# Optimization experiments

Hardware: AMD Instinct MI355X
Metric: run time of the kernel (lower is better)

Reference implementation:

```python
import jax, jax.numpy as jnp
import numpy as np

B, IDF, CDF, H, Wd, L = 16, 128, 256, 128, 128, 64


def setup_inputs() -> dict:
    key = jax.random.key(0)
    k1, k2, k3, k4 = jax.random.split(key, 4)
    x = jax.random.normal(k1, (B, IDF, H, Wd), dtype=jnp.float32)
    context = jax.random.normal(k2, (B, CDF, L), dtype=jnp.float32)
    W = jax.random.normal(k3, (IDF, CDF), dtype=jnp.float32) * 0.02
    mask = jax.random.bernoulli(k4, 0.3, (B, L))
    # guarantee at least one unmasked word per row so the softmax is finite
    mask = mask.at[:, 0].set(False)
    return {"x": x, "context": context, "W": W, "mask": mask}


def reference(x, context, W, mask):
    # x: [B, idf, H, W]  context: [B, cdf, L]  W: [idf, cdf]  mask: [B, L] bool
    b, c, h, w = x.shape
    P = h * w
    l = context.shape[2]
    target = x.reshape(b, c, P)                       # [B, idf, P]
    # Conv1x1 over context (cdf -> idf)
    source = jnp.einsum('oc,bcl->bol', W, context)    # [B, idf, L]
    # QK^T: [B, P, idf] x [B, idf, L] -> [B, P, L]
    attn = jnp.einsum('bip,bil->bpl', target, source)
    attn = attn.reshape(b * P, l)
    # faithful to torch: mask.repeat(P, 1) tiled over the flattened rows
    m = jnp.tile(mask, (P, 1))                        # [B*P, L]
    attn = jnp.where(m, -jnp.inf, attn)
    attn = jax.nn.softmax(attn, axis=1).reshape(b, P, l)
    attnT = jnp.swapaxes(attn, 1, 2)                  # [B, L, P]
    # weighted context: [B, idf, L] x [B, L, P] -> [B, idf, P]
    weight = jnp.einsum('bil,blp->bip', source, attnT).reshape(b, c, h, w)
    attn_out = attnT.reshape(b, l, h, w)
    return weight, attn_out
```

## Files before the change

kernel.cpp:

```cpp
#include <hip/hip_runtime.h>
#include <hip/hip_bf16.h>
#include <hip/hip_fp16.h>

#define NB  16
#define IDF 128
#define CDF 256
#define LL  64
#define PP  16384
#define PXB 256
#define XPITCH 260

typedef _Float16 f16;
typedef _Float16 f16x4 __attribute__((ext_vector_type(4)));
typedef _Float16 f16x8 __attribute__((ext_vector_type(8)));
typedef float    f32x4 __attribute__((ext_vector_type(4)));

__global__ void src_pack_kernel(const float* __restrict__ Wm,
                                const float* __restrict__ ctx,
                                f16* __restrict__ srcF,
                                f16* __restrict__ srcT,
                                const unsigned char* __restrict__ mask_raw,
                                unsigned long long* __restrict__ mbits) {
    if (blockIdx.x == 0) {
        __shared__ int is_u8;
        const int tid = threadIdx.x;
        if (tid == 0) is_u8 = 0;
        if (tid < 16) mbits[tid] = 0ULL;
        __syncthreads();
        unsigned char byt[4];
        #pragma unroll
        for (int q = 0; q < 4; ++q) {
            int k = tid + q * 256;
            byt[q] = mask_raw[k];
            if ((k & 3) != 0 && byt[q] != 0) atomicOr(&is_u8, 1);
        }
        __syncthreads();
        #pragma unroll
        for (int q = 0; q < 4; ++q) {
            int k = tid + q * 256;
            int masked;
            if (is_u8) masked = (byt[q] != 0);
            else       masked = (((const int*)mask_raw)[k] != 0);
            if (masked) atomicOr(&mbits[k >> 6], 1ULL << (unsigned)(k & 63));
        }
    }

    int g = blockIdx.x * 256 + threadIdx.x;
    int l = g & (LL - 1);
    int i = (g >> 6) & (IDF - 1);
    int b = g >> 13;
    const float* wrow = Wm + (size_t)i * CDF;
    const float* ccol = ctx + (size_t)b * CDF * LL + l;
    float s = 0.f;
    #pragma unroll 8
    for (int c = 0; c < CDF; ++c)
        s = fmaf(wrow[c], ccol[(size_t)c * LL], s);
    f16 h = (f16)s;
    srcF[g] = h;
    srcT[((size_t)b * LL + l) * IDF + i] = h;
}

__global__ __launch_bounds__(256, 2)
void attn_mfma_kernel(const float* __restrict__ x,
                      const f16* __restrict__ srcT,
                      const f16* __restrict__ srcF,
                      const unsigned long long* __restrict__ mbits,
                      float* __restrict__ weight,
                      float* __restrict__ attn_out) {
    __shared__ __align__(16) unsigned char s_srcT[LL * 256];
    __shared__ __align__(16) unsigned char s_srcF[IDF * 128];
    __shared__ __align__(16) unsigned char s_u[34816];

    float* s_xpA = (float*)s_u;
    float* s_xpB = (float*)(s_u + 16640);

    const int b    = blockIdx.y;
    const int tid  = threadIdx.x;
    const int wv   = tid >> 6;
    const int lane = tid & 63;
    const int c    = lane & 15;
    const int g    = lane >> 4;
    const int cs   = (c & 7) << 4;

    f16* s_pw = (f16*)s_u + (size_t)wv * (64 * 68);

    const int bxs = (blockIdx.x & 7) * 8 + (blockIdx.x >> 3);
    const int pwb = bxs * PXB;
    const int pww = pwb + wv * 64;
    const float* xb = x + (size_t)b * IDF * PP + pww + c;

    unsigned mlo[4], mhi[4];
    #pragma unroll
    for (int r = 0; r < 4; ++r) {
        unsigned long long m = mbits[4 * g + r];
        mlo[r] = (unsigned)m;
        mhi[r] = (unsigned)(m >> 32);
    }

    float xfa[32], xfb[32];
#define QK_LOAD(BUF, KS)                                                    \
    {   _Pragma("unroll")                                                   \
        for (int pt = 0; pt < 4; ++pt)                                      \
            _Pragma("unroll")                                               \
            for (int j = 0; j < 8; ++j)                                     \
                BUF[pt * 8 + j] =                                           \
                    xb[(size_t)((KS) * 32 + 8 * g + j) * PP + pt * 16];     \
    }

    QK_LOAD(xfa, 0)

    {
        const f16* sT = srcT + (size_t)b * LL * IDF;
        const f16* sF = srcF + (size_t)b * IDF * LL;
        #pragma unroll
        for (int it = 0; it < 4; ++it) {
            int e = (it * 256 + tid) * 8;
            int l = e >> 7, i = e & 127;
            f16x8 v = *reinterpret_cast<const f16x8*>(sT + l * IDF + i);
            *reinterpret_cast<f16x8*>(
                s_srcT + l * 256 + ((i * 2) ^ ((l & 7) << 4))) = v;
        }
        #pragma unroll
        for (int it = 0; it < 4; ++it) {
            int e = (it * 256 + tid) * 8;
            int i = e >> 6, l = e & 63;
            f16x8 v = *reinterpret_cast<const f16x8*>(sF + i * LL + l);
            *reinterpret_cast<f16x8*>(
                s_srcF + i * 128 + ((l * 2) ^ ((i & 7) << 4))) = v;
        }
    }
    __syncthreads();

    f32x4 acc[4][4];
    #pragma unroll
    for (int pt = 0; pt < 4; ++pt)
        #pragma unroll
        for (int nt = 0; nt < 4; ++nt) acc[pt][nt] = (f32x4){0.f, 0.f, 0.f, 0.f};

#define QK_STEP(BUF, KS)                                                    \
    {   f16x8 xa[4];                                                        \
        _Pragma("unroll")                                                   \
        for (int pt = 0; pt < 4; ++pt)                                      \
            _Pragma("unroll")                                               \
            for (int j = 0; j < 8; ++j) xa[pt][j] = (f16)BUF[pt * 8 + j];   \
        _Pragma("unroll")                                                   \
        for (int nt = 0; nt < 4; ++nt) {                                    \
            const f16x8 bt = *reinterpret_cast<const f16x8*>(               \
                s_srcT + (nt * 16 + c) * 256 + (((KS) * 64 + 16 * g) ^ cs));\
            _Pragma("unroll")                                               \
            for (int pt = 0; pt < 4; ++pt)                                  \
                acc[pt][nt] = __builtin_amdgcn_mfma_f32_16x16x32_f16(       \
                    xa[pt], bt, acc[pt][nt], 0, 0, 0);                      \
        } }

    QK_LOAD(xfb, 1)
    QK_STEP(xfa, 0)
    QK_LOAD(xfa, 2)
    QK_STEP(xfb, 1)
    QK_LOAD(xfb, 3)
    QK_STEP(xfa, 2)
    QK_STEP(xfb, 3)

    #pragma unroll
    for (int r = 0; r < 4; ++r) {
        const unsigned m0 = (mlo[r] >> c) & 1u;
        const unsigned m1 = (mlo[r] >> (16 + c)) & 1u;
        const unsigned m2 = (mhi[r] >> c) & 1u;
        const unsigned m3 = (mhi[r] >> (16 + c)) & 1u;
        #pragma unroll
        for (int pt = 0; pt < 4; ++pt) {
            if (m0) acc[pt][0][r] = -INFINITY;
            if (m1) acc[pt][1][r] = -INFINITY;
            if (m2) acc[pt][2][r] = -INFINITY;
            if (m3) acc[pt][3][r] = -INFINITY;
        }
    }
    #pragma unroll
    for (int pt = 0; pt < 4; ++pt) {
        #pragma unroll
        for (int r = 0; r < 4; ++r) {
            float mx = fmaxf(fmaxf(acc[pt][0][r], acc[pt][1][r]),
                             fmaxf(acc[pt][2][r], acc[pt][3][r]));
            mx = fmaxf(mx, __shfl_xor(mx, 1, 64));
            mx = fmaxf(mx, __shfl_xor(mx, 2, 64));
            mx = fmaxf(mx, __shfl_xor(mx, 4, 64));
            mx = fmaxf(mx, __shfl_xor(mx, 8, 64));
            float sum = 0.f;
            #pragma unroll
            for (int nt = 0; nt < 4; ++nt) {
                float e = exp2f((acc[pt][nt][r] - mx) * 1.44269504f);
                acc[pt][nt][r] = e;
                sum += e;
            }
            sum += __shfl_xor(sum, 1, 64);
            sum += __shfl_xor(sum, 2, 64);
            sum += __shfl_xor(sum, 4, 64);
            sum += __shfl_xor(sum, 8, 64);
            const float inv = 1.f / sum;
            #pragma unroll
            for (int nt = 0; nt < 4; ++nt) acc[pt][nt][r] *= inv;
        }
    }

    #pragma unroll
    for (int pt = 0; pt < 4; ++pt)
        #pragma unroll
        for (int nt = 0; nt < 4; ++nt)
            #pragma unroll
            for (int r = 0; r < 4; ++r)
                s_pw[(pt * 16 + 4 * g + r) * 68 + nt * 16 + c] =
                    (f16)acc[pt][nt][r];

    f16x8 pa[4][2];
    #pragma unroll
    for (int pt = 0; pt < 4; ++pt)
        #pragma unroll
        for (int ks = 0; ks < 2; ++ks) {
            const f16* pp = s_pw + (pt * 16 + c) * 68 + ks * 32 + 8 * g;
            f16x4 lo = *reinterpret_cast<const f16x4*>(pp);
            f16x4 hi = *reinterpret_cast<const f16x4*>(pp + 4);
            f16x8 v;
            #pragma unroll
            for (int j = 0; j < 4; ++j) { v[j] = lo[j]; v[4 + j] = hi[j]; }
            pa[pt][ks] = v;
        }

    __syncthreads();

    float* abase = attn_out + (size_t)b * LL * PP + pwb;
    float* wbase = weight + (size_t)b * IDF * PP + pwb;

#define FILL_ATTN(NT, XP)                                                   \
    {   _Pragma("unroll")                                                   \
        for (int pt = 0; pt < 4; ++pt)                                      \
            *reinterpret_cast<f32x4*>(                                      \
                (XP) + c * XPITCH + wv * 64 + pt * 16 + 4 * g) = acc[pt][NT]; }

#define FILL_PV(CH, XP)                                                     \
    {   f32x4 a2[4];                                                        \
        _Pragma("unroll")                                                   \
        for (int pt = 0; pt < 4; ++pt) a2[pt] = (f32x4){0.f, 0.f, 0.f, 0.f};\
        _Pragma("unroll")                                                   \
        for (int ks = 0; ks < 2; ++ks) {                                    \
            const f16x8 sf = *reinterpret_cast<const f16x8*>(               \
                s_srcF + ((CH) * 16 + c) * 128 + ((ks * 64 + 16 * g) ^ cs));\
            _Pragma("unroll")                                               \
            for (int pt = 0; pt < 4; ++pt)                                  \
                a2[pt] = __builtin_amdgcn_mfma_f32_16x16x32_f16(            \
                    pa[pt][ks], sf, a2[pt], 0, 0, 0);                       \
        }                                                                   \
        _Pragma("unroll")                                                   \
        for (int pt = 0; pt < 4; ++pt)                                      \
            *reinterpret_cast<f32x4*>(                                      \
                (XP) + c * XPITCH + wv * 64 + pt * 16 + 4 * g) = a2[pt]; }

#define FILL_CHUNK(K, XP)                                                   \
    {   if ((K) < 4) { FILL_ATTN((K), (XP)) }                               \
        else         { FILL_PV((K) - 4, (XP)) } }

#define STORE_CHUNK(K, XP)                                                  \
    {   float* dst = ((K) < 4)                                              \
            ? (abase + (size_t)((K) * 16) * PP)                             \
            : (wbase + (size_t)(((K) - 4) * 16) * PP);                      \
        _Pragma("unroll")                                                   \
        for (int k2 = 0; k2 < 4; ++k2) {                                    \
            int f = tid + k2 * 256;                                         \
            int row = f >> 6, u = f & 63;                                   \
            f32x4 v = *reinterpret_cast<const f32x4*>(                      \
                (XP) + row * XPITCH + u * 4);                               \
            __builtin_nontemporal_store(v,                                  \
                reinterpret_cast<f32x4*>(dst + (size_t)row * PP + u * 4));  \
        } }

    FILL_CHUNK(0, s_xpA)
    __syncthreads();
    #pragma unroll
    for (int k = 0; k < 12; ++k) {
        float* xp_cur = (k & 1) ? s_xpB : s_xpA;
        float* xp_nxt = (k & 1) ? s_xpA : s_xpB;
        STORE_CHUNK(k, xp_cur)
        if (k < 11) { FILL_CHUNK(k + 1, xp_nxt) }
        if (k < 11) __syncthreads();
    }
}

extern "C" void kernel_launch(void* const* d_in, const int* in_sizes, int n_in,
                              void* d_out, int out_size, void* d_ws, size_t ws_size,
                              hipStream_t stream) {
    const float*         x        = (const float*)d_in[0];
    const float*         ctx      = (const float*)d_in[1];
    const float*         Wm       = (const float*)d_in[2];
    const unsigned char* mask_raw = (const unsigned char*)d_in[3];

    float* weight   = (float*)d_out;
    float* attn_out = weight + (size_t)NB * IDF * PP;

    unsigned long long* mbits = (unsigned long long*)d_ws;
    f16* srcF = (f16*)((char*)d_ws + 4096);
    f16* srcT = srcF + (size_t)NB * IDF * LL;

    src_pack_kernel<<<(NB * IDF * LL) / 256, 256, 0, stream>>>(
        Wm, ctx, srcF, srcT, mask_raw, mbits);

    dim3 grid(PP / PXB, NB);
    attn_mfma_kernel<<<grid, 256, 0, stream>>>(x, srcT, srcF, mbits, weight, attn_out);
}
```

Measured before the change: 77.10 us.

## Process two pixel tiles per block and prefetch second tile's x during stores

Each block now handles two consecutive 256-pixel tiles, which halves the grid and reuses the staged source matrices in LDS. The second tile's x loads are issued in the middle of the first tile's store pipeline, so global reads overlap with the output writes. __syncthreads is replaced by an explicit lgkmcnt wait plus s_barrier, so outstanding global stores are not drained at each barrier. The cost is fewer blocks (512 total), which may hurt occupancy or load balance, and more live registers for the prefetched data.

```diff
diff --git a/kernel.cpp b/kernel.cpp
--- a/kernel.cpp
+++ b/kernel.cpp
@@ -14,6 +14,9 @@
 typedef _Float16 f16x4 __attribute__((ext_vector_type(4)));
 typedef _Float16 f16x8 __attribute__((ext_vector_type(8)));
 typedef float    f32x4 __attribute__((ext_vector_type(4)));
+
+#define BAR() do { asm volatile("s_waitcnt lgkmcnt(0)" ::: "memory"); \
+                   __builtin_amdgcn_s_barrier(); } while (0)
 
 __global__ void src_pack_kernel(const float* __restrict__ Wm,
                                 const float* __restrict__ ctx,
@@ -84,10 +87,10 @@
 
     f16* s_pw = (f16*)s_u + (size_t)wv * (64 * 68);
 
-    const int bxs = (blockIdx.x & 7) * 8 + (blockIdx.x >> 3);
-    const int pwb = bxs * PXB;
-    const int pww = pwb + wv * 64;
-    const float* xb = x + (size_t)b * IDF * PP + pww + c;
+    const int bxs = (blockIdx.x & 7) * 4 + (blockIdx.x >> 3);
+    const int pwb = bxs * (2 * PXB);
+    const float* xb0 = x + (size_t)b * IDF * PP + pwb + wv * 64 + c;
+    const float* xb1 = xb0 + PXB;
 
     unsigned mlo[4], mhi[4];
     #pragma unroll
@@ -98,16 +101,159 @@
     }
 
     float xfa[32], xfb[32];
-#define QK_LOAD(BUF, KS)                                                    \
+    f16x8 xh0[4], xh1[4];
+    f32x4 acc[4][4];
+    f16x8 pa[4][2];
+
+#define QK_LOAD(BUF, KS, XB)                                                \
     {   _Pragma("unroll")                                                   \
         for (int pt = 0; pt < 4; ++pt)                                      \
             _Pragma("unroll")                                               \
             for (int j = 0; j < 8; ++j)                                     \
                 BUF[pt * 8 + j] =                                           \
-                    xb[(size_t)((KS) * 32 + 8 * g + j) * PP + pt * 16];     \
-    }
-
-    QK_LOAD(xfa, 0)
+                    (XB)[(size_t)((KS) * 32 + 8 * g + j) * PP + pt * 16];   \
+    }
+
+#define QK_CONV(BUF, XH)                                                    \
+    {   _Pragma("unroll")                                                   \
+        for (int pt = 0; pt < 4; ++pt)                                      \
+            _Pragma("unroll")                                               \
+            for (int j = 0; j < 8; ++j) XH[pt][j] = (f16)BUF[pt * 8 + j];   \
+    }
+
+#define QK_STEP_H(XH, KS)                                                   \
+    {   _Pragma("unroll")                                                   \
+        for (int nt = 0; nt < 4; ++nt) {                                    \
+            const f16x8 bt = *reinterpret_cast<const f16x8*>(               \
+                s_srcT + (nt * 16 + c) * 256 + (((KS) * 64 + 16 * g) ^ cs));\
+            _Pragma("unroll")                                               \
+            for (int pt = 0; pt < 4; ++pt)                                  \
+                acc[pt][nt] = __builtin_amdgcn_mfma_f32_16x16x32_f16(       \
+                    XH[pt], bt, acc[pt][nt], 0, 0, 0);                      \
+        } }
+
+#define QK_STEP(BUF, KS)                                                    \
+    {   f16x8 xa_[4];                                                       \
+        QK_CONV(BUF, xa_)                                                   \
+        QK_STEP_H(xa_, KS) }
+
+#define ACC_ZERO()                                                          \
+    {   _Pragma("unroll")                                                   \
+        for (int pt = 0; pt < 4; ++pt)                                      \
+            _Pragma("unroll")                                               \
+            for (int nt = 0; nt < 4; ++nt)                                  \
+                acc[pt][nt] = (f32x4){0.f, 0.f, 0.f, 0.f}; }
+
+#define SOFTMAX()                                                           \
+    {   _Pragma("unroll")                                                   \
+        for (int r = 0; r < 4; ++r) {                                       \
+            const unsigned m0 = (mlo[r] >> c) & 1u;                         \
+            const unsigned m1 = (mlo[r] >> (16 + c)) & 1u;                  \
+            const unsigned m2 = (mhi[r] >> c) & 1u;                         \
+            const unsigned m3 = (mhi[r] >> (16 + c)) & 1u;                  \
+            _Pragma("unroll")                                               \
+            for (int pt = 0; pt < 4; ++pt) {                                \
+                if (m0) acc[pt][0][r] = -INFINITY;                          \
+                if (m1) acc[pt][1][r] = -INFINITY;                          \
+                if (m2) acc[pt][2][r] = -INFINITY;                          \
+                if (m3) acc[pt][3][r] = -INFINITY;                          \
+            }                                                               \
+        }                                                                   \
+        _Pragma("unroll")                                                   \
+        for (int pt = 0; pt < 4; ++pt) {                                    \
+            _Pragma("unroll")                                               \
+            for (int r = 0; r < 4; ++r) {                                   \
+                float mx = fmaxf(fmaxf(acc[pt][0][r], acc[pt][1][r]),       \
+                                 fmaxf(acc[pt][2][r], acc[pt][3][r]));      \
+                mx = fmaxf(mx, __shfl_xor(mx, 1, 64));                      \
+                mx = fmaxf(mx, __shfl_xor(mx, 2, 64));                      \
+                mx = fmaxf(mx, __shfl_xor(mx, 4, 64));                      \
+                mx = fmaxf(mx, __shfl_xor(mx, 8, 64));                      \
+                float sum = 0.f;                                            \
+                _Pragma("unroll")                                           \
+                for (int nt = 0; nt < 4; ++nt) {                            \
+                    float e = exp2f((acc[pt][nt][r] - mx) * 1.44269504f);   \
+                    acc[pt][nt][r] = e;                                     \
+                    sum += e;                                               \
+                }                                                           \
+                sum += __shfl_xor(sum, 1, 64);                              \
+                sum += __shfl_xor(sum, 2, 64);                              \
+                sum += __shfl_xor(sum, 4, 64);                              \
+                sum += __shfl_xor(sum, 8, 64);                              \
+                const float inv = 1.f / sum;                                \
+                _Pragma("unroll")                                           \
+                for (int nt = 0; nt < 4; ++nt) acc[pt][nt][r] *= inv;       \
+            }                                                               \
+        } }
+
+#define PROB_EXCHANGE()                                                     \
+    {   _Pragma("unroll")                                                   \
+        for (int pt = 0; pt < 4; ++pt)                                      \
+            _Pragma("unroll")                                               \
+            for (int nt = 0; nt < 4; ++nt)                                  \
+                _Pragma("unroll")                                           \
+                for (int r = 0; r < 4; ++r)                                 \
+                    s_pw[(pt * 16 + 4 * g + r) * 68 + nt * 16 + c] =        \
+                        (f16)acc[pt][nt][r];                                \
+        _Pragma("unroll")                                                   \
+        for (int pt = 0; pt < 4; ++pt)                                      \
+            _Pragma("unroll")                                               \
+            for (int ks = 0; ks < 2; ++ks) {                                \
+                const f16* pp = s_pw + (pt * 16 + c) * 68 + ks * 32 + 8 * g;\
+                f16x4 lo = *reinterpret_cast<const f16x4*>(pp);             \
+                f16x4 hi = *reinterpret_cast<const f16x4*>(pp + 4);         \
+                f16x8 v;                                                    \
+                _Pragma("unroll")                                           \
+                for (int j = 0; j < 4; ++j) { v[j] = lo[j]; v[4+j] = hi[j]; } \
+                pa[pt][ks] = v;                                             \
+            } }
+
+#define FILL_ATTN(NT, XP)                                                   \
+    {   _Pragma("unroll")                                                   \
+        for (int pt = 0; pt < 4; ++pt)                                      \
+            *reinterpret_cast<f32x4*>(                                      \
+                (XP) + c * XPITCH + wv * 64 + pt * 16 + 4 * g) = acc[pt][NT]; }
+
+#define FILL_PV(CH, XP)                                                     \
+    {   f32x4 a2[4];                                                        \
+        _Pragma("unroll")                                                   \
+        for (int pt = 0; pt < 4; ++pt) a2[pt] = (f32x4){0.f, 0.f, 0.f, 0.f};\
+        _Pragma("unroll")                                                   \
+        for (int ks = 0; ks < 2; ++ks) {                                    \
+            const f16x8 sf = *reinterpret_cast<const f16x8*>(               \
+                s_srcF + ((CH) * 16 + c) * 128 + ((ks * 64 + 16 * g) ^ cs));\
+            _Pragma("unroll")                                               \
+            for (int pt = 0; pt < 4; ++pt)                                  \
+                a2[pt] = __builtin_amdgcn_mfma_f32_16x16x32_f16(            \
+                    pa[pt][ks], sf, a2[pt], 0, 0, 0);                       \
+        }                                                                   \
+        _Pragma("unroll")                                                   \
+        for (int pt = 0; pt < 4; ++pt)                                      \
+            *reinterpret_cast<f32x4*>(                                      \
+                (XP) + c * XPITCH + wv * 64 + pt * 16 + 4 * g) = a2[pt]; }
+
+#define FILL_CHUNK(K, XP)                                                   \
+    {   if ((K) < 4) { FILL_ATTN((K), (XP)) }                               \
+        else         { FILL_PV((K) - 4, (XP)) } }
+
+#define STORE_CHUNK(K, XP, AB, WB)                                          \
+    {   float* dst = ((K) < 4)                                              \
+            ? ((AB) + (size_t)((K) * 16) * PP)                              \
+            : ((WB) + (size_t)(((K) - 4) * 16) * PP);                       \
+        _Pragma("unroll")                                                   \
+        for (int k2 = 0; k2 < 4; ++k2) {                                    \
+            int f = tid + k2 * 256;                                         \
+            int row = f >> 6, u = f & 63;                                   \
+            f32x4 v = *reinterpret_cast<const f32x4*>(                      \
+                (XP) + row * XPITCH + u * 4);                               \
+            __builtin_nontemporal_store(v,                                  \
+                reinterpret_cast<f32x4*>(dst + (size_t)row * PP + u * 4));  \
+        } }
+
+#define PIPE_STEP(K, CUR, NXT, AB, WB)                                      \
+    STORE_CHUNK(K, CUR, AB, WB) FILL_CHUNK((K) + 1, NXT) BAR();
+
+    QK_LOAD(xfa, 0, xb0)
 
     {
         const f16* sT = srcT + (size_t)b * LL * IDF;
@@ -129,159 +275,70 @@
                 s_srcF + i * 128 + ((l * 2) ^ ((i & 7) << 4))) = v;
         }
     }
-    __syncthreads();
-
-    f32x4 acc[4][4];
-    #pragma unroll
-    for (int pt = 0; pt < 4; ++pt)
-        #pragma unroll
-        for (int nt = 0; nt < 4; ++nt) acc[pt][nt] = (f32x4){0.f, 0.f, 0.f, 0.f};
-
-#define QK_STEP(BUF, KS)                                                    \
-    {   f16x8 xa[4];                                                        \
-        _Pragma("unroll")                                                   \
-        for (int pt = 0; pt < 4; ++pt)                                      \
-            _Pragma("unroll")                                               \
-            for (int j = 0; j < 8; ++j) xa[pt][j] = (f16)BUF[pt * 8 + j];   \
-        _Pragma("unroll")                                                   \
-        for (int nt = 0; nt < 4; ++nt) {                                    \
-            const f16x8 bt = *reinterpret_cast<const f16x8*>(               \
-                s_srcT + (nt * 16 + c) * 256 + (((KS) * 64 + 16 * g) ^ cs));\
-            _Pragma("unroll")                                               \
-            for (int pt = 0; pt < 4; ++pt)                                  \
-                acc[pt][nt] = __builtin_amdgcn_mfma_f32_16x16x32_f16(       \
-                    xa[pt], bt, acc[pt][nt], 0, 0, 0);                      \
-        } }
-
-    QK_LOAD(xfb, 1)
+    BAR();
+
+    ACC_ZERO()
+    QK_LOAD(xfb, 1, xb0)
     QK_STEP(xfa, 0)
-    QK_LOAD(xfa, 2)
+    QK_LOAD(xfa, 2, xb0)
     QK_STEP(xfb, 1)
-    QK_LOAD(xfb, 3)
+    QK_LOAD(xfb, 3, xb0)
     QK_STEP(xfa, 2)
     QK_STEP(xfb, 3)
-
-    #pragma unroll
-    for (int r = 0; r < 4; ++r) {
-        const unsigned m0 = (mlo[r] >> c) & 1u;
-        const unsigned m1 = (mlo[r] >> (16 + c)) & 1u;
-        const unsigned m2 = (mhi[r] >> c) & 1u;
-        const unsigned m3 = (mhi[r] >> (16 + c)) & 1u;
-        #pragma unroll
-        for (int pt = 0; pt < 4; ++pt) {
-            if (m0) acc[pt][0][r] = -INFINITY;
-            if (m1) acc[pt][1][r] = -INFINITY;
-            if (m2) acc[pt][2][r] = -INFINITY;
-            if (m3) acc[pt][3][r] = -INFINITY;
-        }
-    }
-    #pragma unroll
-    for (int pt = 0; pt < 4; ++pt) {
-        #pragma unroll
-        for (int r = 0; r < 4; ++r) {
-            float mx = fmaxf(fmaxf(acc[pt][0][r], acc[pt][1][r]),
-                             fmaxf(acc[pt][2][r], acc[pt][3][r]));
-            mx = fmaxf(mx, __shfl_xor(mx, 1, 64));
-            mx = fmaxf(mx, __shfl_xor(mx, 2, 64));
-            mx = fmaxf(mx, __shfl_xor(mx, 4, 64));
-            mx = fmaxf(mx, __shfl_xor(mx, 8, 64));
-            float sum = 0.f;
-            #pragma unroll
-            for (int nt = 0; nt < 4; ++nt) {
-                float e = exp2f((acc[pt][nt][r] - mx) * 1.44269504f);
-                acc[pt][nt][r] = e;
-                sum += e;
-            }
-            sum += __shfl_xor(sum, 1, 64);
-            sum += __shfl_xor(sum, 2, 64);
-            sum += __shfl_xor(sum, 4, 64);
-            sum += __shfl_xor(sum, 8, 64);
-            const float inv = 1.f / sum;
-            #pragma unroll
-            for (int nt = 0; nt < 4; ++nt) acc[pt][nt][r] *= inv;
-        }
-    }
-
-    #pragma unroll
-    for (int pt = 0; pt < 4; ++pt)
-        #pragma unroll
-        for (int nt = 0; nt < 4; ++nt)
-            #pragma unroll
-            for (int r = 0; r < 4; ++r)
-                s_pw[(pt * 16 + 4 * g + r) * 68 + nt * 16 + c] =
-                    (f16)acc[pt][nt][r];
-
-    f16x8 pa[4][2];
-    #pragma unroll
-    for (int pt = 0; pt < 4; ++pt)
-        #pragma unroll
-        for (int ks = 0; ks < 2; ++ks) {
-            const f16* pp = s_pw + (pt * 16 + c) * 68 + ks * 32 + 8 * g;
-            f16x4 lo = *reinterpret_cast<const f16x4*>(pp);
-            f16x4 hi = *reinterpret_cast<const f16x4*>(pp + 4);
-            f16x8 v;
-            #pragma unroll
-            for (int j = 0; j < 4; ++j) { v[j] = lo[j]; v[4 + j] = hi[j]; }
-            pa[pt][ks] = v;
-        }
-
-    __syncthreads();
-
-    float* abase = attn_out + (size_t)b * LL * PP + pwb;
-    float* wbase = weight + (size_t)b * IDF * PP + pwb;
-
-#define FILL_ATTN(NT, XP)                                                   \
-    {   _Pragma("unroll")                                                   \
-        for (int pt = 0; pt < 4; ++pt)                                      \
-            *reinterpret_cast<f32x4*>(                                      \
-                (XP) + c * XPITCH + wv * 64 + pt * 16 + 4 * g) = acc[pt][NT]; }
-
-#define FILL_PV(CH, XP)                                                     \
-    {   f32x4 a2[4];                                                        \
-        _Pragma("unroll")                                                   \
-        for (int pt = 0; pt < 4; ++pt) a2[pt] = (f32x4){0.f, 0.f, 0.f, 0.f};\
-        _Pragma("unroll")                                                   \
-        for (int ks = 0; ks < 2; ++ks) {                                    \
-            const f16x8 sf = *reinterpret_cast<const f16x8*>(               \
-                s_srcF + ((CH) * 16 + c) * 128 + ((ks * 64 + 16 * g) ^ cs));\
-            _Pragma("unroll")                                               \
-            for (int pt = 0; pt < 4; ++pt)                                  \
-                a2[pt] = __builtin_amdgcn_mfma_f32_16x16x32_f16(            \
-                    pa[pt][ks], sf, a2[pt], 0, 0, 0);                       \
-        }                                                                   \
-        _Pragma("unroll")                                                   \
-        for (int pt = 0; pt < 4; ++pt)                                      \
-            *reinterpret_cast<f32x4*>(                                      \
-                (XP) + c * XPITCH + wv * 64 + pt * 16 + 4 * g) = a2[pt]; }
-
-#define FILL_CHUNK(K, XP)                                                   \
-    {   if ((K) < 4) { FILL_ATTN((K), (XP)) }                               \
-        else         { FILL_PV((K) - 4, (XP)) } }
-
-#define STORE_CHUNK(K, XP)                                                  \
-    {   float* dst = ((K) < 4)                                              \
-            ? (abase + (size_t)((K) * 16) * PP)                             \
-            : (wbase + (size_t)(((K) - 4) * 16) * PP);                      \
-        _Pragma("unroll")                                                   \
-        for (int k2 = 0; k2 < 4; ++k2) {                                    \
-            int f = tid + k2 * 256;                                         \
-            int row = f >> 6, u = f & 63;                                   \
-            f32x4 v = *reinterpret_cast<const f32x4*>(                      \
-                (XP) + row * XPITCH + u * 4);                               \
-            __builtin_nontemporal_store(v,                                  \
-                reinterpret_cast<f32x4*>(dst + (size_t)row * PP + u * 4));  \
-        } }
+    SOFTMAX()
+    PROB_EXCHANGE()
+    BAR();
+
+    float* abase0 = attn_out + (size_t)b * LL * PP + pwb;
+    float* wbase0 = weight + (size_t)b * IDF * PP + pwb;
+    float* abase1 = abase0 + PXB;
+    float* wbase1 = wbase0 + PXB;
 
     FILL_CHUNK(0, s_xpA)
-    __syncthreads();
-    #pragma unroll
-    for (int k = 0; k < 12; ++k) {
-        float* xp_cur = (k & 1) ? s_xpB : s_xpA;
-        float* xp_nxt = (k & 1) ? s_xpA : s_xpB;
-        STORE_CHUNK(k, xp_cur)
-        if (k < 11) { FILL_CHUNK(k + 1, xp_nxt) }
-        if (k < 11) __syncthreads();
-    }
+    BAR();
+    PIPE_STEP(0, s_xpA, s_xpB, abase0, wbase0)
+    PIPE_STEP(1, s_xpB, s_xpA, abase0, wbase0)
+    PIPE_STEP(2, s_xpA, s_xpB, abase0, wbase0)
+    QK_LOAD(xfa, 0, xb1)
+    QK_LOAD(xfb, 1, xb1)
+    PIPE_STEP(3, s_xpB, s_xpA, abase0, wbase0)
+    PIPE_STEP(4, s_xpA, s_xpB, abase0, wbase0)
+    PIPE_STEP(5, s_xpB, s_xpA, abase0, wbase0)
+    PIPE_STEP(6, s_xpA, s_xpB, abase0, wbase0)
+    QK_CONV(xfa, xh0)
+    QK_CONV(xfb, xh1)
+    QK_LOAD(xfa, 2, xb1)
+    QK_LOAD(xfb, 3, xb1)
+    PIPE_STEP(7, s_xpB, s_xpA, abase0, wbase0)
+    PIPE_STEP(8, s_xpA, s_xpB, abase0, wbase0)
+    PIPE_STEP(9, s_xpB, s_xpA, abase0, wbase0)
+    PIPE_STEP(10, s_xpA, s_xpB, abase0, wbase0)
+    STORE_CHUNK(11, s_xpB, abase0, wbase0)
+    BAR();
+
+    ACC_ZERO()
+    QK_STEP_H(xh0, 0)
+    QK_STEP_H(xh1, 1)
+    QK_STEP(xfa, 2)
+    QK_STEP(xfb, 3)
+    SOFTMAX()
+    PROB_EXCHANGE()
+    BAR();
+
+    FILL_CHUNK(0, s_xpA)
+    BAR();
+    PIPE_STEP(0, s_xpA, s_xpB, abase1, wbase1)
+    PIPE_STEP(1, s_xpB, s_xpA, abase1, wbase1)
+    PIPE_STEP(2, s_xpA, s_xpB, abase1, wbase1)
+    PIPE_STEP(3, s_xpB, s_xpA, abase1, wbase1)
+    PIPE_STEP(4, s_xpA, s_xpB, abase1, wbase1)
+    PIPE_STEP(5, s_xpB, s_xpA, abase1, wbase1)
+    PIPE_STEP(6, s_xpA, s_xpB, abase1, wbase1)
+    PIPE_STEP(7, s_xpB, s_xpA, abase1, wbase1)
+    PIPE_STEP(8, s_xpA, s_xpB, abase1, wbase1)
+    PIPE_STEP(9, s_xpB, s_xpA, abase1, wbase1)
+    PIPE_STEP(10, s_xpA, s_xpB, abase1, wbase1)
+    STORE_CHUNK(11, s_xpB, abase1, wbase1)
 }
 
 extern "C" void kernel_launch(void* const* d_in, const int* in_sizes, int n_in,
@@ -302,6 +359,6 @@
     src_pack_kernel<<<(NB * IDF * LL) / 256, 256, 0, stream>>>(
         Wm, ctx, srcF, srcT, mask_raw, mbits);
 
-    dim3 grid(PP / PXB, NB);
+    dim3 grid(PP / (2 * PXB), NB);
     attn_mfma_kernel<<<grid, 256, 0, stream>>>(x, srcT, srcF, mbits, weight, attn_out);
 }
```

After: 77.78 us. About the same (+0.9%).

## Single-buffer LDS staging and raise occupancy to three blocks per CU

Applied to the files above, without the earlier changes.

Shrinks the shared staging area from a double buffer to a single buffer and shrinks the per-wave probability scratch by staging P in two halves. This lowers LDS per block so launch bounds can request three blocks per CU. It also replaces __syncthreads with a custom barrier that only waits on LDS counters, not global loads or stores. The cost is an extra barrier per output chunk, since fill and store no longer overlap, and tighter register limits that may cause spills.

```diff
diff --git a/kernel.cpp b/kernel.cpp
--- a/kernel.cpp
+++ b/kernel.cpp
@@ -14,6 +14,9 @@
 typedef _Float16 f16x4 __attribute__((ext_vector_type(4)));
 typedef _Float16 f16x8 __attribute__((ext_vector_type(8)));
 typedef float    f32x4 __attribute__((ext_vector_type(4)));
+
+#define BAR() do { asm volatile("s_waitcnt lgkmcnt(0)" ::: "memory"); \
+                   __builtin_amdgcn_s_barrier(); } while (0)
 
 __global__ void src_pack_kernel(const float* __restrict__ Wm,
                                 const float* __restrict__ ctx,
@@ -60,7 +63,7 @@
     srcT[((size_t)b * LL + l) * IDF + i] = h;
 }
 
-__global__ __launch_bounds__(256, 2)
+__global__ __launch_bounds__(256, 3)
 void attn_mfma_kernel(const float* __restrict__ x,
                       const f16* __restrict__ srcT,
                       const f16* __restrict__ srcF,
@@ -69,10 +72,9 @@
                       float* __restrict__ attn_out) {
     __shared__ __align__(16) unsigned char s_srcT[LL * 256];
     __shared__ __align__(16) unsigned char s_srcF[IDF * 128];
-    __shared__ __align__(16) unsigned char s_u[34816];
-
-    float* s_xpA = (float*)s_u;
-    float* s_xpB = (float*)(s_u + 16640);
+    __shared__ __align__(16) unsigned char s_u[17408];
+
+    float* s_xp = (float*)s_u;
 
     const int b    = blockIdx.y;
     const int tid  = threadIdx.x;
@@ -82,7 +84,7 @@
     const int g    = lane >> 4;
     const int cs   = (c & 7) << 4;
 
-    f16* s_pw = (f16*)s_u + (size_t)wv * (64 * 68);
+    f16* s_pw = (f16*)(s_u + (size_t)wv * 4352);
 
     const int bxs = (blockIdx.x & 7) * 8 + (blockIdx.x >> 3);
     const int pwb = bxs * PXB;
@@ -98,6 +100,9 @@
     }
 
     float xfa[32], xfb[32];
+    f32x4 acc[4][4];
+    f16x8 pa[4][2];
+
 #define QK_LOAD(BUF, KS)                                                    \
     {   _Pragma("unroll")                                                   \
         for (int pt = 0; pt < 4; ++pt)                                      \
@@ -107,6 +112,22 @@
                     xb[(size_t)((KS) * 32 + 8 * g + j) * PP + pt * 16];     \
     }
 
+#define QK_STEP(BUF, KS)                                                    \
+    {   f16x8 xa_[4];                                                       \
+        _Pragma("unroll")                                                   \
+        for (int pt = 0; pt < 4; ++pt)                                      \
+            _Pragma("unroll")                                               \
+            for (int j = 0; j < 8; ++j) xa_[pt][j] = (f16)BUF[pt * 8 + j];  \
+        _Pragma("unroll")                                                   \
+        for (int nt = 0; nt < 4; ++nt) {                                    \
+            const f16x8 bt = *reinterpret_cast<const f16x8*>(               \
+                s_srcT + (nt * 16 + c) * 256 + (((KS) * 64 + 16 * g) ^ cs));\
+            _Pragma("unroll")                                               \
+            for (int pt = 0; pt < 4; ++pt)                                  \
+                acc[pt][nt] = __builtin_amdgcn_mfma_f32_16x16x32_f16(       \
+                    xa_[pt], bt, acc[pt][nt], 0, 0, 0);                     \
+        } }
+
     QK_LOAD(xfa, 0)
 
     {
@@ -129,29 +150,12 @@
                 s_srcF + i * 128 + ((l * 2) ^ ((i & 7) << 4))) = v;
         }
     }
-    __syncthreads();
-
-    f32x4 acc[4][4];
+    BAR();
+
     #pragma unroll
     for (int pt = 0; pt < 4; ++pt)
         #pragma unroll
         for (int nt = 0; nt < 4; ++nt) acc[pt][nt] = (f32x4){0.f, 0.f, 0.f, 0.f};
-
-#define QK_STEP(BUF, KS)                                                    \
-    {   f16x8 xa[4];                                                        \
-        _Pragma("unroll")                                                   \
-        for (int pt = 0; pt < 4; ++pt)                                      \
-            _Pragma("unroll")                                               \
-            for (int j = 0; j < 8; ++j) xa[pt][j] = (f16)BUF[pt * 8 + j];   \
-        _Pragma("unroll")                                                   \
-        for (int nt = 0; nt < 4; ++nt) {                                    \
-            const f16x8 bt = *reinterpret_cast<const f16x8*>(               \
-                s_srcT + (nt * 16 + c) * 256 + (((KS) * 64 + 16 * g) ^ cs));\
-            _Pragma("unroll")                                               \
-            for (int pt = 0; pt < 4; ++pt)                                  \
-                acc[pt][nt] = __builtin_amdgcn_mfma_f32_16x16x32_f16(       \
-                    xa[pt], bt, acc[pt][nt], 0, 0, 0);                      \
-        } }
 
     QK_LOAD(xfb, 1)
     QK_STEP(xfa, 0)
@@ -203,40 +207,44 @@
     }
 
     #pragma unroll
-    for (int pt = 0; pt < 4; ++pt)
-        #pragma unroll
-        for (int nt = 0; nt < 4; ++nt)
+    for (int h = 0; h < 2; ++h) {
+        #pragma unroll
+        for (int pl = 0; pl < 2; ++pl) {
+            const int pt = h * 2 + pl;
             #pragma unroll
-            for (int r = 0; r < 4; ++r)
-                s_pw[(pt * 16 + 4 * g + r) * 68 + nt * 16 + c] =
-                    (f16)acc[pt][nt][r];
-
-    f16x8 pa[4][2];
-    #pragma unroll
-    for (int pt = 0; pt < 4; ++pt)
-        #pragma unroll
-        for (int ks = 0; ks < 2; ++ks) {
-            const f16* pp = s_pw + (pt * 16 + c) * 68 + ks * 32 + 8 * g;
-            f16x4 lo = *reinterpret_cast<const f16x4*>(pp);
-            f16x4 hi = *reinterpret_cast<const f16x4*>(pp + 4);
-            f16x8 v;
+            for (int nt = 0; nt < 4; ++nt)
+                #pragma unroll
+                for (int r = 0; r < 4; ++r)
+                    s_pw[(pl * 16 + 4 * g + r) * 68 + nt * 16 + c] =
+                        (f16)acc[pt][nt][r];
+        }
+        #pragma unroll
+        for (int pl = 0; pl < 2; ++pl) {
+            const int pt = h * 2 + pl;
             #pragma unroll
-            for (int j = 0; j < 4; ++j) { v[j] = lo[j]; v[4 + j] = hi[j]; }
-            pa[pt][ks] = v;
-        }
-
-    __syncthreads();
+            for (int ks = 0; ks < 2; ++ks) {
+                const f16* pp = s_pw + (pl * 16 + c) * 68 + ks * 32 + 8 * g;
+                f16x4 lo = *reinterpret_cast<const f16x4*>(pp);
+                f16x4 hi = *reinterpret_cast<const f16x4*>(pp + 4);
+                f16x8 v;
+                #pragma unroll
+                for (int j = 0; j < 4; ++j) { v[j] = lo[j]; v[4 + j] = hi[j]; }
+                pa[pt][ks] = v;
+            }
+        }
+    }
+    BAR();
 
     float* abase = attn_out + (size_t)b * LL * PP + pwb;
     float* wbase = weight + (size_t)b * IDF * PP + pwb;
 
-#define FILL_ATTN(NT, XP)                                                   \
+#define FILL_ATTN(NT)                                                       \
     {   _Pragma("unroll")                                                   \
         for (int pt = 0; pt < 4; ++pt)                                      \
             *reinterpret_cast<f32x4*>(                                      \
-                (XP) + c * XPITCH + wv * 64 + pt * 16 + 4 * g) = acc[pt][NT]; }
-
-#define FILL_PV(CH, XP)                                                     \
+                s_xp + c * XPITCH + wv * 64 + pt * 16 + 4 * g) = acc[pt][NT]; }
+
+#define FILL_PV(CH)                                                         \
     {   f32x4 a2[4];                                                        \
         _Pragma("unroll")                                                   \
         for (int pt = 0; pt < 4; ++pt) a2[pt] = (f32x4){0.f, 0.f, 0.f, 0.f};\
@@ -252,13 +260,9 @@
         _Pragma("unroll")                                                   \
         for (int pt = 0; pt < 4; ++pt)                                      \
             *reinterpret_cast<f32x4*>(                                      \
-                (XP) + c * XPITCH + wv * 64 + pt * 16 + 4 * g) = a2[pt]; }
-
-#define FILL_CHUNK(K, XP)                                                   \
-    {   if ((K) < 4) { FILL_ATTN((K), (XP)) }                               \
-        else         { FILL_PV((K) - 4, (XP)) } }
-
-#define STORE_CHUNK(K, XP)                                                  \
+                s_xp + c * XPITCH + wv * 64 + pt * 16 + 4 * g) = a2[pt]; }
+
+#define STORE_CHUNK(K)                                                      \
     {   float* dst = ((K) < 4)                                              \
             ? (abase + (size_t)((K) * 16) * PP)                             \
             : (wbase + (size_t)(((K) - 4) * 16) * PP);                      \
@@ -267,21 +271,21 @@
             int f = tid + k2 * 256;                                         \
             int row = f >> 6, u = f & 63;                                   \
             f32x4 v = *reinterpret_cast<const f32x4*>(                      \
-                (XP) + row * XPITCH + u * 4);                               \
+                s_xp + row * XPITCH + u * 4);                               \
             __builtin_nontemporal_store(v,                                  \
                 reinterpret_cast<f32x4*>(dst + (size_t)row * PP + u * 4));  \
         } }
 
-    FILL_CHUNK(0, s_xpA)
-    __syncthreads();
-    #pragma unroll
-    for (int k = 0; k < 12; ++k) {
-        float* xp_cur = (k & 1) ? s_xpB : s_xpA;
-        float* xp_nxt = (k & 1) ? s_xpA : s_xpB;
-        STORE_CHUNK(k, xp_cur)
-        if (k < 11) { FILL_CHUNK(k + 1, xp_nxt) }
-        if (k < 11) __syncthreads();
-    }
+#define CHUNK(K)                                                            \
+    {   if ((K) < 4) { FILL_ATTN(K) } else { FILL_PV((K) - 4) }             \
+        BAR();                                                              \
+        STORE_CHUNK(K)                                                      \
+        BAR(); }
+
+    CHUNK(0)  CHUNK(1)  CHUNK(2)  CHUNK(3)
+    CHUNK(4)  CHUNK(5)  CHUNK(6)  CHUNK(7)
+    CHUNK(8)  CHUNK(9)  CHUNK(10)
+    { FILL_PV(7) BAR(); STORE_CHUNK(11) }
 }
 
 extern "C" void kernel_launch(void* const* d_in, const int* in_sizes, int n_in,
```

Measured after the change: 72.75 us. 1.06x faster.
